# Kernel tuning notes

Measured on AMD Instinct MI355X. Metric: run time of the kernel, lower is better.

## Reference

```python
import jax, jax.numpy as jnp
import numpy as np

B, C_IN, C_OUT, F, K = 4, 64, 64, 50000, 16
BN_EPS = 1e-5


def setup_inputs() -> dict:
    key = jax.random.key(0)
    k1, k2, k3, k4 = jax.random.split(key, 4)
    fea = jax.random.normal(k1, (B, C_IN, F), dtype=jnp.float32)
    ring_n = jax.random.randint(k2, (B, F, K), 0, F, dtype=jnp.int64)
    # Conv1d(kernel_size=1) weight [out, in] and bias [out]
    W = jax.random.normal(k3, (C_OUT, C_IN), dtype=jnp.float32) / np.sqrt(C_IN)
    b = jax.random.normal(k4, (C_OUT,), dtype=jnp.float32) * 0.01
    gamma = jnp.ones((C_OUT,), dtype=jnp.float32)
    beta = jnp.zeros((C_OUT,), dtype=jnp.float32)
    return {"fea": fea, "ring_n": ring_n, "W": W, "b": b, "gamma": gamma, "beta": beta}


def reference(fea, ring_n, W, b, gamma, beta):
    # Note: original torch code overwrites the cat result, so only the
    # NEIGHBOR features are summed (center face excluded).
    def gather_sum(f, r):  # f: [C, F], r: [F, K]
        return f[:, r].sum(axis=-1)  # [C, F, K] -> [C, F]

    summed = jax.vmap(gather_sum)(fea, ring_n)  # [B, C_in, F]
    # 1x1 conv == channel matmul
    y = jnp.einsum("oc,bcf->bof", W, summed) + b[None, :, None]  # [B, C_out, F]
    # BatchNorm1d (training mode): stats over (batch, faces) per channel
    mean = y.mean(axis=(0, 2), keepdims=True)
    var = y.var(axis=(0, 2), keepdims=True)  # biased, as torch BN uses for normalization
    y = (y - mean) * jax.lax.rsqrt(var + BN_EPS)
    y = y * gamma[None, :, None] + beta[None, :, None]
    return jax.nn.relu(y)
```

## Files before the change

### kernel.cpp

```cpp
#include <hip/hip_runtime.h>
#include <hip/hip_bf16.h>
#include <stdint.h>

#define Bn 4
#define Cn 64
#define Fn 50000
#define Kn 16
#define NTOT (Bn*Fn)
#define EPS 1e-5f

typedef unsigned short u16;
typedef unsigned int u32;

__device__ __forceinline__ u16 f2bf(float x) {
  __hip_bfloat16 h = __float2bfloat16(x);
  return *reinterpret_cast<u16*>(&h);
}
__device__ __forceinline__ u32 pack2(float a, float b) {
  return (u32)f2bf(a) | ((u32)f2bf(b) << 16);
}

__global__ __launch_bounds__(256) void k1_wgemm(
    const float* __restrict__ fea, const float* __restrict__ W,
    u32* __restrict__ Gt) {
  const int b = blockIdx.y;
  const int f0 = blockIdx.x * 128;
  __shared__ float a_s[64][132];
  __shared__ float w_s[64][68];
  const int t = threadIdx.x;
  {
    const float4* W4 = (const float4*)W;
    #pragma unroll
    for (int jj = 0; jj < 4; ++jj) {
      int l = jj * 256 + t;
      float4 v = W4[l];
      int o = l >> 4;
      int c = (l & 15) << 2;
      w_s[c][o] = v.x; w_s[c+1][o] = v.y; w_s[c+2][o] = v.z; w_s[c+3][o] = v.w;
    }
  }
  {
    const float* fb = fea + ((size_t)b * Cn) * Fn + f0;
    #pragma unroll
    for (int jj = 0; jj < 8; ++jj) {
      int l = jj * 256 + t;
      int c = l >> 5;
      int fi = (l & 31) << 2;
      float4 v = make_float4(0.f, 0.f, 0.f, 0.f);
      if (f0 + fi < Fn) v = *(const float4*)(fb + (size_t)c * Fn + fi);
      *(float4*)&a_s[c][fi] = v;
    }
  }
  __syncthreads();
  const int sg = t >> 6;
  const int fl = t & 63;
  float acc[2][16];
  #pragma unroll
  for (int j = 0; j < 2; j++)
    #pragma unroll
    for (int i = 0; i < 16; i++) acc[j][i] = 0.f;
  const int o0 = sg << 4;
  #pragma unroll 4
  for (int c = 0; c < 64; c++) {
    float4 w0 = *(float4*)&w_s[c][o0];
    float4 w1 = *(float4*)&w_s[c][o0 + 4];
    float4 w2 = *(float4*)&w_s[c][o0 + 8];
    float4 w3 = *(float4*)&w_s[c][o0 + 12];
    float2 av = *(float2*)&a_s[c][fl << 1];
    float wv[16] = {w0.x,w0.y,w0.z,w0.w, w1.x,w1.y,w1.z,w1.w,
                    w2.x,w2.y,w2.z,w2.w, w3.x,w3.y,w3.z,w3.w};
    #pragma unroll
    for (int i = 0; i < 16; i++) {
      acc[0][i] = fmaf(av.x, wv[i], acc[0][i]);
      acc[1][i] = fmaf(av.y, wv[i], acc[1][i]);
    }
  }
  u32* gdst = Gt + ((size_t)(b * 4 + sg) * Fn + f0 + (fl << 1)) * 8;
  #pragma unroll
  for (int j = 0; j < 2; j++) {
    int f = f0 + (fl << 1) + j;
    if (f < Fn) {
      uint4 u0, u1;
      u0.x = pack2(acc[j][0], acc[j][1]);   u0.y = pack2(acc[j][2], acc[j][3]);
      u0.z = pack2(acc[j][4], acc[j][5]);   u0.w = pack2(acc[j][6], acc[j][7]);
      u1.x = pack2(acc[j][8], acc[j][9]);   u1.y = pack2(acc[j][10], acc[j][11]);
      u1.z = pack2(acc[j][12], acc[j][13]); u1.w = pack2(acc[j][14], acc[j][15]);
      *(uint4*)(gdst + (size_t)j * 8) = u0;
      *(uint4*)(gdst + (size_t)j * 8 + 4) = u1;
    }
  }
}

template<int WRITE_BF16>
__global__ __launch_bounds__(256) void k2_gather(
    const u32* __restrict__ Gt, const int* __restrict__ ring,
    const float* __restrict__ bias, u32* __restrict__ Y, float* __restrict__ outF,
    float* __restrict__ gsum, float* __restrict__ gsum2) {
  const int bid = blockIdx.x;
  const int combo = bid & 15;
  const int ft = bid >> 4;
  const int b = combo >> 2;
  const int seg = combo & 3;
  const int t = threadIdx.x;
  const int face_l = t >> 1;
  const int half = t & 1;
  const int fa = ft * 128 + face_l;
  const bool valid = fa < Fn;

  __shared__ float y_s[128][17];
  __shared__ float rs[16][17];
  __shared__ float rs2[16][17];

  float acc[8];
  #pragma unroll
  for (int i = 0; i < 8; i++) acc[i] = 0.f;

  const int c0 = seg * 16 + half * 8;
  float bv[8];
  #pragma unroll
  for (int i = 0; i < 8; i++) bv[i] = bias[c0 + i];

  if (valid) {
    const int4* rp = (const int4*)(ring + ((size_t)b * Fn + fa) * Kn);
    int4 i0 = rp[0], i1 = rp[1], i2 = rp[2], i3 = rp[3];
    int idx[16] = {i0.x,i0.y,i0.z,i0.w, i1.x,i1.y,i1.z,i1.w,
                   i2.x,i2.y,i2.z,i2.w, i3.x,i3.y,i3.z,i3.w};
    const uint4* Gs = (const uint4*)(Gt + (size_t)(b * 4 + seg) * Fn * 8);
    uint4 v[8], w[8];
    #pragma unroll
    for (int k = 0; k < 8; k++) v[k] = Gs[(size_t)idx[k] * 2 + half];
    #pragma unroll
    for (int k = 0; k < 8; k++) w[k] = Gs[(size_t)idx[8 + k] * 2 + half];
    #pragma unroll
    for (int k = 0; k < 8; k++) {
      u32 uu[4] = {v[k].x, v[k].y, v[k].z, v[k].w};
      #pragma unroll
      for (int p = 0; p < 4; p++) {
        acc[2*p]   += __uint_as_float(uu[p] << 16);
        acc[2*p+1] += __uint_as_float(uu[p] & 0xffff0000u);
      }
    }
    #pragma unroll
    for (int k = 0; k < 8; k++) {
      u32 uu[4] = {w[k].x, w[k].y, w[k].z, w[k].w};
      #pragma unroll
      for (int p = 0; p < 4; p++) {
        acc[2*p]   += __uint_as_float(uu[p] << 16);
        acc[2*p+1] += __uint_as_float(uu[p] & 0xffff0000u);
      }
    }
  }
  #pragma unroll
  for (int i = 0; i < 8; i++) acc[i] = valid ? acc[i] + bv[i] : 0.f;
  #pragma unroll
  for (int i = 0; i < 8; i++) y_s[face_l][half * 8 + i] = acc[i];
  __syncthreads();

  if (WRITE_BF16) {
    const int fp = t & 63;
    const int chb = t >> 6;
    const int fa2 = ft * 64 + fp;
    if (fa2 * 2 < Fn) {
      #pragma unroll
      for (int j = 0; j < 4; j++) {
        int ch = chb * 4 + j;
        u32 pv = pack2(y_s[fp * 2][ch], y_s[fp * 2 + 1][ch]);
        Y[((size_t)b * 64 + seg * 16 + ch) * (Fn / 2) + fa2] = pv;
      }
    }
  } else {
    const int fl2 = t & 127;
    const int chb = t >> 7;
    if (ft * 128 + fl2 < Fn) {
      float* ob = outF + ((size_t)b * 64 + seg * 16 + chb * 8) * Fn + ft * 128 + fl2;
      #pragma unroll
      for (int j = 0; j < 8; j++) ob[(size_t)j * Fn] = y_s[fl2][chb * 8 + j];
    }
  }

  {
    const int ch = t & 15, part = t >> 4;
    float s = 0.f, s2 = 0.f;
    #pragma unroll
    for (int i = 0; i < 8; i++) {
      float v = y_s[part * 8 + i][ch];
      s += v; s2 += v * v;
    }
    rs[part][ch] = s; rs2[part][ch] = s2;
  }
  __syncthreads();
  if (t < 16) {
    float s = 0.f;
    #pragma unroll
    for (int p = 0; p < 16; p++) s += rs[p][t];
    atomicAdd(&gsum[seg * 16 + t], s);
  } else if (t < 32) {
    const int ch = t - 16;
    float s2 = 0.f;
    #pragma unroll
    for (int p = 0; p < 16; p++) s2 += rs2[p][ch];
    atomicAdd(&gsum2[seg * 16 + ch], s2);
  }
}

__global__ void k3_stats(const float* __restrict__ gsum, const float* __restrict__ gsum2,
                         const float* __restrict__ gamma, const float* __restrict__ beta,
                         float* __restrict__ ab) {
  int o = threadIdx.x;
  if (o < 64) {
    float inv = 1.0f / (float)NTOT;
    float mean = gsum[o] * inv;
    float var = gsum2[o] * inv - mean * mean;
    float r = rsqrtf(var + EPS);
    float a = gamma[o] * r;
    ab[o] = a;
    ab[64 + o] = beta[o] - mean * a;
  }
}

__global__ __launch_bounds__(256) void k4_norm_bf(const u32* __restrict__ Y,
                                                  const float* __restrict__ ab,
                                                  float* __restrict__ out) {
  int i = blockIdx.x * 256 + threadIdx.x;
  int cglob = i / 12500;
  int c = cglob & 63;
  float a = ab[c], cc = ab[64 + c];
  uint2 u = ((const uint2*)Y)[i];
  float4 v;
  v.x = __uint_as_float(u.x << 16);
  v.y = __uint_as_float(u.x & 0xffff0000u);
  v.z = __uint_as_float(u.y << 16);
  v.w = __uint_as_float(u.y & 0xffff0000u);
  v.x = fmaxf(fmaf(v.x, a, cc), 0.f);
  v.y = fmaxf(fmaf(v.y, a, cc), 0.f);
  v.z = fmaxf(fmaf(v.z, a, cc), 0.f);
  v.w = fmaxf(fmaf(v.w, a, cc), 0.f);
  ((float4*)out)[i] = v;
}

__global__ __launch_bounds__(256) void k4_norm_f32(float* __restrict__ out,
                                                   const float* __restrict__ ab) {
  int i = blockIdx.x * 256 + threadIdx.x;
  int o = (i / (Fn / 4)) & 63;
  float a = ab[o], c = ab[64 + o];
  float4 v = ((float4*)out)[i];
  v.x = fmaxf(fmaf(v.x, a, c), 0.f);
  v.y = fmaxf(fmaf(v.y, a, c), 0.f);
  v.z = fmaxf(fmaf(v.z, a, c), 0.f);
  v.w = fmaxf(fmaf(v.w, a, c), 0.f);
  ((float4*)out)[i] = v;
}

extern "C" void kernel_launch(void* const* d_in, const int* in_sizes, int n_in,
                              void* d_out, int out_size, void* d_ws, size_t ws_size,
                              hipStream_t stream) {
  const float* fea   = (const float*)d_in[0];
  const int*   ring  = (const int*)d_in[1];
  const float* W     = (const float*)d_in[2];
  const float* bias  = (const float*)d_in[3];
  const float* gamma = (const float*)d_in[4];
  const float* beta  = (const float*)d_in[5];
  float* out = (float*)d_out;

  u32* Gt = (u32*)d_ws;
  const size_t gtBytes = (size_t)Bn * 4 * Fn * 8 * 4;
  const size_t yBytes  = (size_t)Bn * 64 * (Fn / 2) * 4;
  const bool bf16y = ws_size >= gtBytes + yBytes + 1024;

  u32* Y = (u32*)((char*)d_ws + gtBytes);
  float* gsum  = bf16y ? (float*)((char*)d_ws + gtBytes + yBytes)
                       : (float*)((char*)d_ws + gtBytes);
  float* gsum2 = gsum + 64;
  float* ab    = gsum + 128;

  hipMemsetAsync(gsum, 0, 2 * 64 * sizeof(float), stream);
  k1_wgemm<<<dim3((Fn + 127) / 128, Bn), 256, 0, stream>>>(fea, W, Gt);
  const int ftiles = (Fn + 127) / 128;
  if (bf16y) {
    k2_gather<1><<<dim3(ftiles * 16), 256, 0, stream>>>(Gt, ring, bias, Y, out, gsum, gsum2);
    k3_stats<<<1, 64, 0, stream>>>(gsum, gsum2, gamma, beta, ab);
    k4_norm_bf<<<dim3((Bn * 64 * (Fn / 2) / 2) / 256), 256, 0, stream>>>(Y, ab, out);
  } else {
    k2_gather<0><<<dim3(ftiles * 16), 256, 0, stream>>>(Gt, ring, bias, Y, out, gsum, gsum2);
    k3_stats<<<1, 64, 0, stream>>>(gsum, gsum2, gamma, beta, ab);
    k4_norm_f32<<<dim3((Bn * Cn * Fn / 4) / 256), 256, 0, stream>>>(out, ab);
  }
}
```

Before: 211.4 us.

## Use bf16 MFMA for channel GEMM and widen gather rows to 32 channels

Replaces the scalar FP32 FMA channel GEMM with bf16 16x16x32 MFMA instructions. The input features are staged as packed bf16 in shared memory, and the weights are held in register fragments. The intermediate G layout changes from 4 segments of 16 channels to 2 segments of 32 channels, so each gathered neighbour row is 64 bytes. The gather kernel now uses 4 threads per face over 64-face tiles, which means fewer, wider random gathers. The price is bf16 rounding of the inputs and weights before the GEMM, a precision loss that did not exist before.

Result: slower. 243.7 us (+15.3%).

```diff
diff --git a/kernel.cpp b/kernel.cpp
--- a/kernel.cpp
+++ b/kernel.cpp
@@ -8,9 +8,12 @@
 #define Kn 16
 #define NTOT (Bn*Fn)
 #define EPS 1e-5f
+#define ROWB 136
 
 typedef unsigned short u16;
 typedef unsigned int u32;
+typedef __attribute__((ext_vector_type(8))) short short8;
+typedef __attribute__((ext_vector_type(4))) float f32x4;
 
 __device__ __forceinline__ u16 f2bf(float x) {
   __hip_bfloat16 h = __float2bfloat16(x);
@@ -20,73 +23,82 @@
   return (u32)f2bf(a) | ((u32)f2bf(b) << 16);
 }
 
-__global__ __launch_bounds__(256) void k1_wgemm(
+__global__ __launch_bounds__(256) void k1_mfma(
     const float* __restrict__ fea, const float* __restrict__ W,
     u32* __restrict__ Gt) {
   const int b = blockIdx.y;
-  const int f0 = blockIdx.x * 128;
-  __shared__ float a_s[64][132];
-  __shared__ float w_s[64][68];
+  const int f0 = blockIdx.x * 256;
   const int t = threadIdx.x;
+  const int l = t & 63;
+  const int quad = l >> 4;
+  __shared__ char a_s[256 * ROWB];
+
+  short8 afr[4][2];
+  #pragma unroll
+  for (int ot = 0; ot < 4; ot++) {
+    #pragma unroll
+    for (int kk = 0; kk < 2; kk++) {
+      const float* wr = W + (ot * 16 + (l & 15)) * 64 + kk * 32 + quad * 8;
+      float4 wa = *(const float4*)wr;
+      float4 wb = *(const float4*)(wr + 4);
+      union { short8 v; u32 u[4]; } fr;
+      fr.u[0] = pack2(wa.x, wa.y); fr.u[1] = pack2(wa.z, wa.w);
+      fr.u[2] = pack2(wb.x, wb.y); fr.u[3] = pack2(wb.z, wb.w);
+      afr[ot][kk] = fr.v;
+    }
+  }
+
   {
-    const float4* W4 = (const float4*)W;
-    #pragma unroll
-    for (int jj = 0; jj < 4; ++jj) {
-      int l = jj * 256 + t;
-      float4 v = W4[l];
-      int o = l >> 4;
-      int c = (l & 15) << 2;
-      w_s[c][o] = v.x; w_s[c+1][o] = v.y; w_s[c+2][o] = v.z; w_s[c+3][o] = v.w;
-    }
-  }
-  {
-    const float* fb = fea + ((size_t)b * Cn) * Fn + f0;
-    #pragma unroll
-    for (int jj = 0; jj < 8; ++jj) {
-      int l = jj * 256 + t;
-      int c = l >> 5;
-      int fi = (l & 31) << 2;
-      float4 v = make_float4(0.f, 0.f, 0.f, 0.f);
-      if (f0 + fi < Fn) v = *(const float4*)(fb + (size_t)c * Fn + fi);
-      *(float4*)&a_s[c][fi] = v;
+    const float* fb_ = fea + ((size_t)b * Cn) * Fn;
+    #pragma unroll
+    for (int i = 0; i < 32; i++) {
+      int cp = (t >> 6) + 4 * (i >> 2);
+      int fl = (t & 63) + 64 * (i & 3);
+      int fg = f0 + fl;
+      float va = 0.f, vb = 0.f;
+      if (fg < Fn) {
+        va = fb_[(size_t)(2 * cp) * Fn + fg];
+        vb = fb_[(size_t)(2 * cp + 1) * Fn + fg];
+      }
+      *(u32*)(a_s + fl * ROWB + 4 * cp) = pack2(va, vb);
     }
   }
   __syncthreads();
-  const int sg = t >> 6;
-  const int fl = t & 63;
-  float acc[2][16];
-  #pragma unroll
-  for (int j = 0; j < 2; j++)
-    #pragma unroll
-    for (int i = 0; i < 16; i++) acc[j][i] = 0.f;
-  const int o0 = sg << 4;
-  #pragma unroll 4
-  for (int c = 0; c < 64; c++) {
-    float4 w0 = *(float4*)&w_s[c][o0];
-    float4 w1 = *(float4*)&w_s[c][o0 + 4];
-    float4 w2 = *(float4*)&w_s[c][o0 + 8];
-    float4 w3 = *(float4*)&w_s[c][o0 + 12];
-    float2 av = *(float2*)&a_s[c][fl << 1];
-    float wv[16] = {w0.x,w0.y,w0.z,w0.w, w1.x,w1.y,w1.z,w1.w,
-                    w2.x,w2.y,w2.z,w2.w, w3.x,w3.y,w3.z,w3.w};
-    #pragma unroll
-    for (int i = 0; i < 16; i++) {
-      acc[0][i] = fmaf(av.x, wv[i], acc[0][i]);
-      acc[1][i] = fmaf(av.y, wv[i], acc[1][i]);
-    }
-  }
-  u32* gdst = Gt + ((size_t)(b * 4 + sg) * Fn + f0 + (fl << 1)) * 8;
-  #pragma unroll
-  for (int j = 0; j < 2; j++) {
-    int f = f0 + (fl << 1) + j;
-    if (f < Fn) {
-      uint4 u0, u1;
-      u0.x = pack2(acc[j][0], acc[j][1]);   u0.y = pack2(acc[j][2], acc[j][3]);
-      u0.z = pack2(acc[j][4], acc[j][5]);   u0.w = pack2(acc[j][6], acc[j][7]);
-      u1.x = pack2(acc[j][8], acc[j][9]);   u1.y = pack2(acc[j][10], acc[j][11]);
-      u1.z = pack2(acc[j][12], acc[j][13]); u1.w = pack2(acc[j][14], acc[j][15]);
-      *(uint4*)(gdst + (size_t)j * 8) = u0;
-      *(uint4*)(gdst + (size_t)j * 8 + 4) = u1;
+
+  const int wv = t >> 6;
+  f32x4 acc[4][4];
+  #pragma unroll
+  for (int ot = 0; ot < 4; ot++)
+    #pragma unroll
+    for (int ft = 0; ft < 4; ft++) acc[ot][ft] = (f32x4){0.f, 0.f, 0.f, 0.f};
+
+  #pragma unroll
+  for (int ft = 0; ft < 4; ft++) {
+    int frow = wv * 64 + ft * 16 + (l & 15);
+    char* p = a_s + frow * ROWB + quad * 16;
+    union { short8 v; uint2 u[2]; } b0, b1;
+    b0.u[0] = *(uint2*)(p);      b0.u[1] = *(uint2*)(p + 8);
+    b1.u[0] = *(uint2*)(p + 64); b1.u[1] = *(uint2*)(p + 72);
+    #pragma unroll
+    for (int ot = 0; ot < 4; ot++) {
+      acc[ot][ft] = __builtin_amdgcn_mfma_f32_16x16x32_bf16(afr[ot][0], b0.v, acc[ot][ft], 0, 0, 0);
+      acc[ot][ft] = __builtin_amdgcn_mfma_f32_16x16x32_bf16(afr[ot][1], b1.v, acc[ot][ft], 0, 0, 0);
+    }
+  }
+
+  #pragma unroll
+  for (int ot = 0; ot < 4; ot++) {
+    int s2 = ot >> 1;
+    int ch0 = (ot & 1) * 16 + quad * 4;
+    #pragma unroll
+    for (int ft = 0; ft < 4; ft++) {
+      int fg = f0 + wv * 64 + ft * 16 + (l & 15);
+      if (fg < Fn) {
+        uint2 pv;
+        pv.x = pack2(acc[ot][ft][0], acc[ot][ft][1]);
+        pv.y = pack2(acc[ot][ft][2], acc[ot][ft][3]);
+        *(uint2*)(Gt + ((size_t)(b * 2 + s2) * Fn + fg) * 16 + (ch0 >> 1)) = pv;
+      }
     }
   }
 }
@@ -97,40 +109,37 @@
     const float* __restrict__ bias, u32* __restrict__ Y, float* __restrict__ outF,
     float* __restrict__ gsum, float* __restrict__ gsum2) {
   const int bid = blockIdx.x;
-  const int combo = bid & 15;
-  const int ft = bid >> 4;
-  const int b = combo >> 2;
-  const int seg = combo & 3;
+  const int combo = bid & 7;
+  const int ft = bid >> 3;
+  const int b = combo >> 1;
+  const int s2 = combo & 1;
   const int t = threadIdx.x;
-  const int face_l = t >> 1;
-  const int half = t & 1;
-  const int fa = ft * 128 + face_l;
+  const int face = t >> 2;
+  const int q = t & 3;
+  const int f0 = ft * 64;
+  const int fa = f0 + face;
   const bool valid = fa < Fn;
 
-  __shared__ float y_s[128][17];
-  __shared__ float rs[16][17];
-  __shared__ float rs2[16][17];
+  __shared__ float y_s[64][33];
+  __shared__ float rs[8][33];
+  __shared__ float rs2[8][33];
 
   float acc[8];
   #pragma unroll
   for (int i = 0; i < 8; i++) acc[i] = 0.f;
-
-  const int c0 = seg * 16 + half * 8;
-  float bv[8];
-  #pragma unroll
-  for (int i = 0; i < 8; i++) bv[i] = bias[c0 + i];
+  const int chl0 = q * 8;
 
   if (valid) {
     const int4* rp = (const int4*)(ring + ((size_t)b * Fn + fa) * Kn);
     int4 i0 = rp[0], i1 = rp[1], i2 = rp[2], i3 = rp[3];
     int idx[16] = {i0.x,i0.y,i0.z,i0.w, i1.x,i1.y,i1.z,i1.w,
                    i2.x,i2.y,i2.z,i2.w, i3.x,i3.y,i3.z,i3.w};
-    const uint4* Gs = (const uint4*)(Gt + (size_t)(b * 4 + seg) * Fn * 8);
+    const uint4* Gs = (const uint4*)(Gt + (size_t)combo * Fn * 16);
     uint4 v[8], w[8];
     #pragma unroll
-    for (int k = 0; k < 8; k++) v[k] = Gs[(size_t)idx[k] * 2 + half];
-    #pragma unroll
-    for (int k = 0; k < 8; k++) w[k] = Gs[(size_t)idx[8 + k] * 2 + half];
+    for (int k = 0; k < 8; k++) v[k] = Gs[(size_t)idx[k] * 4 + q];
+    #pragma unroll
+    for (int k = 0; k < 8; k++) w[k] = Gs[(size_t)idx[8 + k] * 4 + q];
     #pragma unroll
     for (int k = 0; k < 8; k++) {
       u32 uu[4] = {v[k].x, v[k].y, v[k].z, v[k].w};
@@ -151,55 +160,54 @@
     }
   }
   #pragma unroll
-  for (int i = 0; i < 8; i++) acc[i] = valid ? acc[i] + bv[i] : 0.f;
-  #pragma unroll
-  for (int i = 0; i < 8; i++) y_s[face_l][half * 8 + i] = acc[i];
+  for (int i = 0; i < 8; i++)
+    acc[i] = valid ? acc[i] + bias[s2 * 32 + chl0 + i] : 0.f;
+  #pragma unroll
+  for (int i = 0; i < 8; i++) y_s[face][chl0 + i] = acc[i];
   __syncthreads();
 
   if (WRITE_BF16) {
-    const int fp = t & 63;
-    const int chb = t >> 6;
-    const int fa2 = ft * 64 + fp;
+    const int fp = t & 31, cb = t >> 5;
+    const int fa2 = ft * 32 + fp;
     if (fa2 * 2 < Fn) {
       #pragma unroll
       for (int j = 0; j < 4; j++) {
-        int ch = chb * 4 + j;
-        u32 pv = pack2(y_s[fp * 2][ch], y_s[fp * 2 + 1][ch]);
-        Y[((size_t)b * 64 + seg * 16 + ch) * (Fn / 2) + fa2] = pv;
+        int ch = cb * 4 + j;
+        Y[((size_t)b * 64 + s2 * 32 + ch) * (Fn / 2) + fa2] =
+            pack2(y_s[fp * 2][ch], y_s[fp * 2 + 1][ch]);
       }
     }
   } else {
-    const int fl2 = t & 127;
-    const int chb = t >> 7;
-    if (ft * 128 + fl2 < Fn) {
-      float* ob = outF + ((size_t)b * 64 + seg * 16 + chb * 8) * Fn + ft * 128 + fl2;
-      #pragma unroll
-      for (int j = 0; j < 8; j++) ob[(size_t)j * Fn] = y_s[fl2][chb * 8 + j];
+    const int fl2 = t & 63, cb = t >> 6;
+    if (f0 + fl2 < Fn) {
+      float* ob = outF + ((size_t)b * 64 + s2 * 32 + cb * 8) * Fn + f0 + fl2;
+      #pragma unroll
+      for (int j = 0; j < 8; j++) ob[(size_t)j * Fn] = y_s[fl2][cb * 8 + j];
     }
   }
 
   {
-    const int ch = t & 15, part = t >> 4;
-    float s = 0.f, s2 = 0.f;
+    const int ch = t & 31, part = t >> 5;
+    float s = 0.f, s2v = 0.f;
     #pragma unroll
     for (int i = 0; i < 8; i++) {
       float v = y_s[part * 8 + i][ch];
-      s += v; s2 += v * v;
-    }
-    rs[part][ch] = s; rs2[part][ch] = s2;
+      s += v; s2v += v * v;
+    }
+    rs[part][ch] = s; rs2[part][ch] = s2v;
   }
   __syncthreads();
-  if (t < 16) {
+  if (t < 32) {
     float s = 0.f;
     #pragma unroll
-    for (int p = 0; p < 16; p++) s += rs[p][t];
-    atomicAdd(&gsum[seg * 16 + t], s);
-  } else if (t < 32) {
-    const int ch = t - 16;
-    float s2 = 0.f;
-    #pragma unroll
-    for (int p = 0; p < 16; p++) s2 += rs2[p][ch];
-    atomicAdd(&gsum2[seg * 16 + ch], s2);
+    for (int p = 0; p < 8; p++) s += rs[p][t];
+    atomicAdd(&gsum[s2 * 32 + t], s);
+  } else if (t < 64) {
+    const int ch = t - 32;
+    float s = 0.f;
+    #pragma unroll
+    for (int p = 0; p < 8; p++) s += rs2[p][ch];
+    atomicAdd(&gsum2[s2 * 32 + ch], s);
   }
 }
 
@@ -263,7 +271,7 @@
   float* out = (float*)d_out;
 
   u32* Gt = (u32*)d_ws;
-  const size_t gtBytes = (size_t)Bn * 4 * Fn * 8 * 4;
+  const size_t gtBytes = (size_t)Bn * 2 * Fn * 16 * 4;
   const size_t yBytes  = (size_t)Bn * 64 * (Fn / 2) * 4;
   const bool bf16y = ws_size >= gtBytes + yBytes + 1024;
 
@@ -274,14 +282,14 @@
   float* ab    = gsum + 128;
 
   hipMemsetAsync(gsum, 0, 2 * 64 * sizeof(float), stream);
-  k1_wgemm<<<dim3((Fn + 127) / 128, Bn), 256, 0, stream>>>(fea, W, Gt);
-  const int ftiles = (Fn + 127) / 128;
+  k1_mfma<<<dim3((Fn + 255) / 256, Bn), 256, 0, stream>>>(fea, W, Gt);
+  const int ftiles = (Fn + 63) / 64;
   if (bf16y) {
-    k2_gather<1><<<dim3(ftiles * 16), 256, 0, stream>>>(Gt, ring, bias, Y, out, gsum, gsum2);
+    k2_gather<1><<<dim3(ftiles * 8), 256, 0, stream>>>(Gt, ring, bias, Y, out, gsum, gsum2);
     k3_stats<<<1, 64, 0, stream>>>(gsum, gsum2, gamma, beta, ab);
     k4_norm_bf<<<dim3((Bn * 64 * (Fn / 2) / 2) / 256), 256, 0, stream>>>(Y, ab, out);
   } else {
-    k2_gather<0><<<dim3(ftiles * 16), 256, 0, stream>>>(Gt, ring, bias, Y, out, gsum, gsum2);
+    k2_gather<0><<<dim3(ftiles * 8), 256, 0, stream>>>(Gt, ring, bias, Y, out, gsum, gsum2);
     k3_stats<<<1, 64, 0, stream>>>(gsum, gsum2, gamma, beta, ab);
     k4_norm_f32<<<dim3((Bn * Cn * Fn / 4) / 256), 256, 0, stream>>>(out, ab);
   }
```
